# Kernel optimization log

Hardware: AMD Instinct MI355X
Metric: run time of the kernel (lower is better)

Reference implementation:

```python
import jax, jax.numpy as jnp
import numpy as np

B, S, D, H, F, E = 4, 1024, 1024, 16, 4096, 8
HD = D // H  # head dim


def setup_inputs() -> dict:
    key = jax.random.key(0)
    ks = jax.random.split(key, 8)
    p = lambda k, shp: jax.random.normal(k, shp, jnp.float32) * 0.02
    return {
        "x": jax.random.normal(ks[0], (B, S, D), jnp.float32),
        "mask": jnp.ones((B, S), jnp.int32),
        "in_proj_w": p(ks[1], (3 * D, D)),
        "in_proj_b": jnp.zeros((3 * D,), jnp.float32),
        "out_proj_w": p(ks[2], (D, D)),
        "out_proj_b": jnp.zeros((D,), jnp.float32),
        "ln1_g": jnp.ones((D,), jnp.float32),
        "ln1_b": jnp.zeros((D,), jnp.float32),
        "ln2_g": jnp.ones((D,), jnp.float32),
        "ln2_b": jnp.zeros((D,), jnp.float32),
        "gate_w": p(ks[3], (E, D)),
        "gate_b": jnp.zeros((E,), jnp.float32),
        "w1": p(ks[4], (E, F, D)),
        "b1": jnp.zeros((E, F), jnp.float32),
        "w2": p(ks[5], (E, D, F)),
        "b2": jnp.zeros((E, D), jnp.float32),
    }


def _layernorm(x, g, b, eps=1e-5):
    m = x.mean(-1, keepdims=True)
    v = ((x - m) ** 2).mean(-1, keepdims=True)
    return (x - m) / jnp.sqrt(v + eps) * g + b


def _mha(x, key_pad, in_proj_w, in_proj_b, out_proj_w, out_proj_b):
    # combined QKV projection as in torch nn.MultiheadAttention
    qkv = x @ in_proj_w.T + in_proj_b  # (B,S,3D)
    q, k, v = jnp.split(qkv, 3, axis=-1)
    def heads(t):
        return t.reshape(B, S, H, HD).transpose(0, 2, 1, 3)  # (B,H,S,HD)
    q, k, v = heads(q), heads(k), heads(v)
    scores = jnp.einsum("bhqd,bhkd->bhqk", q, k) / jnp.sqrt(jnp.float32(HD))
    scores = jnp.where(key_pad[:, None, None, :], -1e30, scores)
    attn = jax.nn.softmax(scores, axis=-1)
    out = jnp.einsum("bhqk,bhkd->bhqd", attn, v)  # (B,H,S,HD)
    out = out.transpose(0, 2, 1, 3).reshape(B, S, D)
    return out @ out_proj_w.T + out_proj_b


def _moe(x, gate_w, gate_b, w1, b1, w2, b2):
    logits = x @ gate_w.T + gate_b            # (B,S,E)
    probs = jax.nn.softmax(logits, axis=-1)
    # dense all-expert FFN (faithful to original: every expert computed)
    h = jax.nn.relu(jnp.einsum("bsd,efd->bsef", x, w1) + b1)   # (B,S,E,F)
    all_out = jnp.einsum("bsef,edf->bsed", h, w2) + b2          # (B,S,E,D)
    top_vals, top_idx = jax.lax.top_k(probs, 2)                 # (B,S,2)
    weights = top_vals / (top_vals.sum(-1, keepdims=True) + 1e-9)
    sel = jnp.take_along_axis(all_out, top_idx[..., None], axis=2)  # (B,S,2,D)
    return (sel * weights[..., None]).sum(axis=2)


def reference(x, mask, in_proj_w, in_proj_b, out_proj_w, out_proj_b,
              ln1_g, ln1_b, ln2_g, ln2_b, gate_w, gate_b, w1, b1, w2, b2):
    key_pad = mask == 0  # (B,S) bool
    attn_out = _mha(x, key_pad, in_proj_w, in_proj_b, out_proj_w, out_proj_b)
    x1 = _layernorm(x + attn_out, ln1_g, ln1_b)
    ff = _moe(x1, gate_w, gate_b, w1, b1, w2, b2)
    return _layernorm(x1 + ff, ln2_g, ln2_b)
```

## Files before the change

kernel.cpp:

```cpp
#include <hip/hip_runtime.h>

typedef __attribute__((ext_vector_type(8))) short bf16x8;
typedef __attribute__((ext_vector_type(4))) float f32x4;

#define DEV __device__ __forceinline__

static constexpr int Bb = 4, Sq = 1024, Dd = 1024, Hh = 16, HDd = 64, Ff = 4096, Ee = 8;
static constexpr int Nn = Bb * Sq;
static constexpr int TD = 3 * Dd;
static constexpr int PMAX = 2 * Nn + Ee * 256;

DEV unsigned short f2bf(float x) {
  union { float f; unsigned u; } c; c.f = x;
  unsigned r = c.u + 0x7FFFu + ((c.u >> 16) & 1u);
  return (unsigned short)(r >> 16);
}
DEV float bf2f(unsigned short u) {
  union { unsigned u; float f; } c; c.u = ((unsigned)u) << 16; return c.f;
}

typedef const __attribute__((address_space(1))) unsigned int* gas_t;
typedef __attribute__((address_space(3))) unsigned int* las_t;
DEV void gload16(const void* g, void* l) {
  __builtin_amdgcn_global_load_lds((gas_t)g, (las_t)l, 16, 0, 0);
}

__global__ __launch_bounds__(256) void cvt_kernel(const float* __restrict__ in,
                                                  unsigned short* __restrict__ out) {
  int i = blockIdx.x * 256 + threadIdx.x;
  const float4 a = *(const float4*)(in + (size_t)i * 8);
  const float4 b = *(const float4*)(in + (size_t)i * 8 + 4);
  union { uint4 u; unsigned short s[8]; } pk;
  pk.s[0] = f2bf(a.x); pk.s[1] = f2bf(a.y); pk.s[2] = f2bf(a.z); pk.s[3] = f2bf(a.w);
  pk.s[4] = f2bf(b.x); pk.s[5] = f2bf(b.y); pk.s[6] = f2bf(b.z); pk.s[7] = f2bf(b.w);
  *(uint4*)(out + (size_t)i * 8) = pk.u;
}

DEV void xcd_swz(int& bx, int& by, int gx, int gy) {
  const int nwg = gx * gy;
  int orig = by * gx + bx;
  int q = nwg >> 3, r = nwg & 7;
  int xcd = orig & 7, lin = orig >> 3;
  int wg = (xcd < r ? xcd * (q + 1) : r * (q + 1) + (xcd - r) * q) + lin;
  bx = wg / gy; by = wg % gy;
}

__global__ __launch_bounds__(512) void gemm8p_up(
    const unsigned short* __restrict__ A, const unsigned short* __restrict__ Bw,
    const float* __restrict__ bias, unsigned short* __restrict__ o0,
    const int* __restrict__ poff) {
  constexpr int K = Dd;
  constexpr int NT = K / 64;
  int bx = blockIdx.x, by = blockIdx.y;
  xcd_swz(bx, by, gridDim.x, gridDim.y);
  const int m0 = bx * 256;
  if (m0 >= poff[Ee]) return;
  int e = 0;
#pragma unroll
  for (int k = 1; k < Ee; ++k) if (m0 >= poff[k]) e = k;
  const int n0 = by * 256;
  const unsigned short* Bptr = Bw + (size_t)e * Ff * K;
  const float* biasptr = bias + e * Ff;

  __shared__ __align__(128) unsigned short As[2 * 256 * 64];
  __shared__ __align__(128) unsigned short Bs[2 * 256 * 64];

  const int tid = threadIdx.x;
  const int lane = tid & 63, wid = tid >> 6;
  const int aw = wid & 1, bw = wid >> 1;
  const int lr = lane & 15, lk = lane >> 4;

  const char* aS[2][2]; const char* bS[2][2]; int dOf[2];
#pragma unroll
  for (int it = 0; it < 2; ++it) {
    int b = it * 8192 + tid * 16;
    int r = b >> 7;
    int colb = (b & 127) ^ ((r & 7) << 4);
#pragma unroll
    for (int h = 0; h < 2; ++h) {
      aS[h][it] = (const char*)(A + (size_t)(m0 + h * 128 + r) * K) + colb;
      bS[h][it] = (const char*)(Bptr + (size_t)(n0 + h * 128 + r) * K) + colb;
    }
    dOf[it] = it * 8192 + wid * 1024;
  }
  int aO[2][2][4], bO[2][2][2];
#pragma unroll
  for (int h = 0; h < 2; ++h)
#pragma unroll
    for (int ks = 0; ks < 2; ++ks) {
#pragma unroll
      for (int mi = 0; mi < 4; ++mi) {
        int ra = h * 128 + aw * 64 + mi * 16 + lr;
        aO[h][ks][mi] = ra * 64 + (((ks * 4 + lk) ^ (ra & 7)) << 3);
      }
#pragma unroll
      for (int ni = 0; ni < 2; ++ni) {
        int rb = h * 128 + bw * 32 + ni * 16 + lr;
        bO[h][ks][ni] = rb * 64 + (((ks * 4 + lk) ^ (rb & 7)) << 3);
      }
    }

  f32x4 acc[4][4][2] = {};

  auto ST_A = [&](int t, int h) {
    int buf = t & 1;
#pragma unroll
    for (int it = 0; it < 2; ++it)
      gload16(aS[h][it] + (size_t)t * 128, (char*)As + buf * 32768 + h * 16384 + dOf[it]);
  };
  auto ST_B = [&](int t, int h) {
    int buf = t & 1;
#pragma unroll
    for (int it = 0; it < 2; ++it)
      gload16(bS[h][it] + (size_t)t * 128, (char*)Bs + buf * 32768 + h * 16384 + dOf[it]);
  };

  ST_A(0, 0); ST_B(0, 0); ST_B(0, 1); ST_A(0, 1);

  for (int t = 0; t < NT; ++t) {
    const unsigned short* Ab = As + (t & 1) * 16384;
    const unsigned short* Bb = Bs + (t & 1) * 16384;
#pragma unroll
    for (int p = 0; p < 4; ++p) {
      const int ah = p >> 1, bh = p & 1;
      if (t + 1 < NT) {
        if (p == 0)      ST_A(t + 1, 0);
        else if (p == 1) ST_B(t + 1, 0);
        else if (p == 2) ST_B(t + 1, 1);
        else             ST_A(t + 1, 1);
        asm volatile("s_waitcnt vmcnt(6)" ::: "memory");
      } else {
        if (p == 0)      asm volatile("s_waitcnt vmcnt(4)" ::: "memory");
        else if (p == 1) asm volatile("s_waitcnt vmcnt(2)" ::: "memory");
        else             asm volatile("s_waitcnt vmcnt(0)" ::: "memory");
      }
      __builtin_amdgcn_sched_barrier(0);
      asm volatile("s_barrier" ::: "memory");
      __builtin_amdgcn_sched_barrier(0);
      bf16x8 af[2][4], bf[2][2];
#pragma unroll
      for (int ks = 0; ks < 2; ++ks) {
#pragma unroll
        for (int mi = 0; mi < 4; ++mi) af[ks][mi] = *(const bf16x8*)&Ab[aO[ah][ks][mi]];
#pragma unroll
        for (int ni = 0; ni < 2; ++ni) bf[ks][ni] = *(const bf16x8*)&Bb[bO[bh][ks][ni]];
      }
      __builtin_amdgcn_s_setprio(1);
#pragma unroll
      for (int ks = 0; ks < 2; ++ks)
#pragma unroll
        for (int mi = 0; mi < 4; ++mi)
#pragma unroll
          for (int ni = 0; ni < 2; ++ni)
            acc[p][mi][ni] = __builtin_amdgcn_mfma_f32_16x16x32_bf16(af[ks][mi], bf[ks][ni], acc[p][mi][ni], 0, 0, 0);
      __builtin_amdgcn_s_setprio(0);
    }
  }

#pragma unroll
  for (int p = 0; p < 4; ++p)
#pragma unroll
    for (int ni = 0; ni < 2; ++ni) {
      const int col = n0 + (p & 1) * 128 + bw * 32 + ni * 16 + lr;
      const float bv = biasptr[col];
#pragma unroll
      for (int mi = 0; mi < 4; ++mi)
#pragma unroll
        for (int i = 0; i < 4; ++i) {
          const int row = m0 + (p >> 1) * 128 + aw * 64 + mi * 16 + lk * 4 + i;
          float v = acc[p][mi][ni][i] + bv;
          o0[(size_t)row * Ff + col] = f2bf(fmaxf(v, 0.f));
        }
    }
}

template <int EPI, int BM, int BN>
__global__ __launch_bounds__(256) void gemm_bt(
    const unsigned short* __restrict__ A, const unsigned short* __restrict__ Bw,
    const float* __restrict__ bias, void* __restrict__ o0, void* __restrict__ o1,
    void* __restrict__ o2, int M, int Ncols, int K,
    const int* __restrict__ poff) {
  constexpr int NA = BM / 64, NB = BN / 64;
  constexpr int L = NA + NB;
  constexpr int WM = BM / 2, WN = BN / 2;
  constexpr int MI = WM / 16, NI = WN / 16;
  constexpr int ATILE = BM * 32;
  constexpr int BTILE = BN * 32;

  int bx = blockIdx.x, by = blockIdx.y;
  xcd_swz(bx, by, gridDim.x, gridDim.y);
  const int m0 = bx * BM;
  int e = 0;
  if constexpr (EPI == 3) {
    if (m0 >= poff[Ee]) return;
#pragma unroll
    for (int k = 1; k < Ee; ++k) if (m0 >= poff[k]) e = k;
  } else {
    if (m0 >= M) return;
  }
  const int n0 = by * BN;
  const unsigned short* Bptr = Bw + (size_t)e * Ncols * K;
  const float* biasptr = bias + e * Ncols;

  __shared__ __align__(128) unsigned short As[3 * ATILE];
  __shared__ __align__(128) unsigned short Bs[3 * BTILE];

  const int tid = threadIdx.x;
  const int lane = tid & 63, wid = tid >> 6;
  const int wm = wid >> 1, wn = wid & 1;
  const int lr = lane & 15, lk = lane >> 4;

  const char* aSrc[NA]; const char* bSrc[NB];
  int aDf[NA], bDf[NB];
#pragma unroll
  for (int it = 0; it < NA; ++it) {
    int b = it * 4096 + tid * 16;
    int r = b >> 6;
    int colb = (b & 63) ^ (((r >> 1) & 3) << 4);
    aSrc[it] = (const char*)(A + (size_t)(m0 + r) * K) + colb;
    aDf[it] = it * 4096 + wid * 1024;
  }
#pragma unroll
  for (int it = 0; it < NB; ++it) {
    int b = it * 4096 + tid * 16;
    int r = b >> 6;
    int colb = (b & 63) ^ (((r >> 1) & 3) << 4);
    bSrc[it] = (const char*)(Bptr + (size_t)(n0 + r) * K) + colb;
    bDf[it] = it * 4096 + wid * 1024;
  }
  int aOff[MI], bOff[NI];
#pragma unroll
  for (int i = 0; i < MI; ++i) {
    int ra = wm * WM + i * 16 + lr;
    aOff[i] = ra * 32 + ((lk ^ ((ra >> 1) & 3)) << 3);
  }
#pragma unroll
  for (int i = 0; i < NI; ++i) {
    int rb = wn * WN + i * 16 + lr;
    bOff[i] = rb * 32 + ((lk ^ ((rb >> 1) & 3)) << 3);
  }

  auto STAGE = [&](int t, int buf) {
#pragma unroll
    for (int it = 0; it < NA; ++it)
      gload16(aSrc[it] + (size_t)t * 64, (char*)As + buf * (ATILE * 2) + aDf[it]);
#pragma unroll
    for (int it = 0; it < NB; ++it)
      gload16(bSrc[it] + (size_t)t * 64, (char*)Bs + buf * (BTILE * 2) + bDf[it]);
  };

  f32x4 acc[MI][NI] = {};
  const int NT = K >> 5;

  STAGE(0, 0);
  STAGE(1, 1);
  int cb = 0, sb = 2;
  for (int t = 0; t < NT; ++t) {
    if (t + 1 < NT) {
      if constexpr (L == 4)      asm volatile("s_waitcnt vmcnt(4)" ::: "memory");
      else if constexpr (L == 3) asm volatile("s_waitcnt vmcnt(3)" ::: "memory");
      else                       asm volatile("s_waitcnt vmcnt(2)" ::: "memory");
    } else {
      asm volatile("s_waitcnt vmcnt(0)" ::: "memory");
    }
    __builtin_amdgcn_sched_barrier(0);
    __builtin_amdgcn_s_barrier();
    __builtin_amdgcn_sched_barrier(0);
    if (t + 2 < NT) STAGE(t + 2, sb);
    const unsigned short* Ab = As + cb * ATILE;
    const unsigned short* Bb2 = Bs + cb * BTILE;
    bf16x8 af[MI], bfv[NI];
#pragma unroll
    for (int mi = 0; mi < MI; ++mi) af[mi] = *(const bf16x8*)&Ab[aOff[mi]];
#pragma unroll
    for (int ni = 0; ni < NI; ++ni) bfv[ni] = *(const bf16x8*)&Bb2[bOff[ni]];
#pragma unroll
    for (int mi = 0; mi < MI; ++mi)
#pragma unroll
      for (int ni = 0; ni < NI; ++ni)
        acc[mi][ni] = __builtin_amdgcn_mfma_f32_16x16x32_bf16(af[mi], bfv[ni], acc[mi][ni], 0, 0, 0);
    cb = (cb == 2) ? 0 : cb + 1;
    sb = (sb == 2) ? 0 : sb + 1;
  }

#pragma unroll
  for (int ni = 0; ni < NI; ++ni) {
    const int col = n0 + wn * WN + ni * 16 + lr;
    const float bv = biasptr[col];
#pragma unroll
    for (int mi = 0; mi < MI; ++mi) {
#pragma unroll
      for (int i = 0; i < 4; ++i) {
        const int mloc = wm * WM + mi * 16 + lk * 4 + i;
        float v = acc[mi][ni][i] + bv;
        if constexpr (EPI == 0) {
          int t = m0 + mloc;
          int which = col >> 10, jj = col & 1023, hh = jj >> 6, hd = jj & 63;
          int bb = t >> 10, s = t & 1023;
          unsigned short* dst = (which == 0) ? (unsigned short*)o0
                              : (which == 1) ? (unsigned short*)o1 : (unsigned short*)o2;
          dst[((size_t)(bb * Hh + hh) * Sq + s) * HDd + hd] = f2bf(v);
        } else if constexpr (EPI == 1) {
          ((float*)o0)[(size_t)(m0 + mloc) * Dd + col] = v;
        } else {
          ((unsigned short*)o0)[(size_t)(m0 + mloc) * Dd + col] = f2bf(v);
        }
      }
    }
  }
}

__global__ __launch_bounds__(256) void attn_kernel(
    const unsigned short* __restrict__ qb, const unsigned short* __restrict__ kb,
    const unsigned short* __restrict__ vb, const int* __restrict__ mask,
    unsigned short* __restrict__ attnb) {
  const int qt = blockIdx.x, h = blockIdx.y, b = blockIdx.z;
  const unsigned short* Q = qb + (size_t)(b * Hh + h) * Sq * HDd;
  const unsigned short* Kg = kb + (size_t)(b * Hh + h) * Sq * HDd;
  const unsigned short* Vg = vb + (size_t)(b * Hh + h) * Sq * HDd;

  __shared__ unsigned short Qs[64 * 72], Ks[64 * 72], Vt[64 * 72], Ps[64 * 72];
  __shared__ float Ssm[64 * 65];
  __shared__ float mS[64], lS[64], aS[64];
  __shared__ int mk[64];

  const int tid = threadIdx.x, lane = tid & 63, wid = tid >> 6;
  const int lr = lane & 15, lk = lane >> 4;

#pragma unroll
  for (int it = 0; it < 2; ++it) {
    int c = tid + it * 256; int r = c >> 3, kc = (c & 7) * 8;
    *(uint4*)&Qs[r * 72 + kc] = *(const uint4*)(Q + (size_t)(qt * 64 + r) * 64 + kc);
  }
  if (tid < 64) { mS[tid] = -1e30f; lS[tid] = 0.f; }

  f32x4 oacc[4] = {};

  for (int kt = 0; kt < 16; ++kt) {
    __syncthreads();
#pragma unroll
    for (int it = 0; it < 2; ++it) {
      int c = tid + it * 256; int r = c >> 3, kc = (c & 7) * 8;
      *(uint4*)&Ks[r * 72 + kc] = *(const uint4*)(Kg + (size_t)(kt * 64 + r) * 64 + kc);
    }
    {
      int kk = tid >> 2, hg = (tid & 3) * 16;
      union { uint4 u[2]; unsigned short s[16]; } tv;
      tv.u[0] = *(const uint4*)(Vg + (size_t)(kt * 64 + kk) * 64 + hg);
      tv.u[1] = *(const uint4*)(Vg + (size_t)(kt * 64 + kk) * 64 + hg + 8);
#pragma unroll
      for (int j = 0; j < 16; ++j) Vt[(hg + j) * 72 + kk] = tv.s[j];
    }
    if (tid < 64) mk[tid] = mask[b * Sq + kt * 64 + tid];
    __syncthreads();

    f32x4 sacc[4] = {};
#pragma unroll
    for (int ks = 0; ks < 2; ++ks) {
      bf16x8 aq = *(const bf16x8*)&Qs[(wid * 16 + lr) * 72 + ks * 32 + lk * 8];
#pragma unroll
      for (int ni = 0; ni < 4; ++ni) {
        bf16x8 bk = *(const bf16x8*)&Ks[(ni * 16 + lr) * 72 + ks * 32 + lk * 8];
        sacc[ni] = __builtin_amdgcn_mfma_f32_16x16x32_bf16(aq, bk, sacc[ni], 0, 0, 0);
      }
    }
#pragma unroll
    for (int ni = 0; ni < 4; ++ni)
#pragma unroll
      for (int i = 0; i < 4; ++i) {
        int r = wid * 16 + lk * 4 + i, cc = ni * 16 + lr;
        float v = sacc[ni][i] * 0.125f;
        if (mk[cc] == 0) v = -1e30f;
        Ssm[r * 65 + cc] = v;
      }
    __syncthreads();
    {
      int r = tid >> 2, cg = (tid & 3) * 16;
      float xv[16];
#pragma unroll
      for (int j = 0; j < 16; ++j) xv[j] = Ssm[r * 65 + cg + j];
      float mx = xv[0];
#pragma unroll
      for (int j = 1; j < 16; ++j) mx = fmaxf(mx, xv[j]);
      mx = fmaxf(mx, __shfl_xor(mx, 1));
      mx = fmaxf(mx, __shfl_xor(mx, 2));
      float mprev = mS[r];
      float mnew = fmaxf(mprev, mx);
      float sum = 0.f;
      union { uint4 u[2]; unsigned short s[16]; } pb;
#pragma unroll
      for (int j = 0; j < 16; ++j) {
        float pv = expf(xv[j] - mnew);
        sum += pv; pb.s[j] = f2bf(pv);
      }
      sum += __shfl_xor(sum, 1);
      sum += __shfl_xor(sum, 2);
      *(uint4*)&Ps[r * 72 + cg] = pb.u[0];
      *(uint4*)&Ps[r * 72 + cg + 8] = pb.u[1];
      if ((tid & 3) == 0) {
        float alpha = expf(mprev - mnew);
        mS[r] = mnew; aS[r] = alpha; lS[r] = lS[r] * alpha + sum;
      }
    }
    __syncthreads();
#pragma unroll
    for (int ni = 0; ni < 4; ++ni)
#pragma unroll
      for (int i = 0; i < 4; ++i)
        oacc[ni][i] *= aS[wid * 16 + lk * 4 + i];
#pragma unroll
    for (int ks = 0; ks < 2; ++ks) {
      bf16x8 ap = *(const bf16x8*)&Ps[(wid * 16 + lr) * 72 + ks * 32 + lk * 8];
#pragma unroll
      for (int ni = 0; ni < 4; ++ni) {
        bf16x8 bv = *(const bf16x8*)&Vt[(ni * 16 + lr) * 72 + ks * 32 + lk * 8];
        oacc[ni] = __builtin_amdgcn_mfma_f32_16x16x32_bf16(ap, bv, oacc[ni], 0, 0, 0);
      }
    }
  }
  __syncthreads();
#pragma unroll
  for (int ni = 0; ni < 4; ++ni)
#pragma unroll
    for (int i = 0; i < 4; ++i) {
      int r = wid * 16 + lk * 4 + i;
      int q = qt * 64 + r;
      float v = oacc[ni][i] / lS[r];
      attnb[((size_t)(b * Sq + q)) * Dd + h * 64 + ni * 16 + lr] = f2bf(v);
    }
}

__global__ __launch_bounds__(256) void ln1_route_kernel(
    const float* __restrict__ a, const float* __restrict__ b2,
    const float* __restrict__ g, const float* __restrict__ beta,
    const float* __restrict__ gw, const float* __restrict__ gb,
    float* __restrict__ outf, unsigned short* __restrict__ outb,
    int* __restrict__ cnt, int* __restrict__ tokslot, float* __restrict__ wtok) {
  const int t = blockIdx.x, tid = threadIdx.x;
  float4 v = *(const float4*)(a + (size_t)t * Dd + tid * 4);
  {
    float4 u = *(const float4*)(b2 + (size_t)t * Dd + tid * 4);
    v.x += u.x; v.y += u.y; v.z += u.z; v.w += u.w;
  }
  const int lane = tid & 63, wid = tid >> 6;
  float s = v.x + v.y + v.z + v.w;
  for (int sh = 1; sh < 64; sh <<= 1) s += __shfl_xor(s, sh);
  __shared__ float red[4], red2[4];
  __shared__ float gred[4 * Ee];
  if (lane == 0) red[wid] = s;
  __syncthreads();
  float mean = (red[0] + red[1] + red[2] + red[3]) * (1.f / Dd);
  float dx = v.x - mean, dy = v.y - mean, dz = v.z - mean, dw = v.w - mean;
  float q = dx * dx + dy * dy + dz * dz + dw * dw;
  for (int sh = 1; sh < 64; sh <<= 1) q += __shfl_xor(q, sh);
  if (lane == 0) red2[wid] = q;
  __syncthreads();
  float var = (red2[0] + red2[1] + red2[2] + red2[3]) * (1.f / Dd);
  float rstd = rsqrtf(var + 1e-5f);
  float4 gg = *(const float4*)(g + tid * 4);
  float4 bbv = *(const float4*)(beta + tid * 4);
  float4 o;
  o.x = dx * rstd * gg.x + bbv.x;
  o.y = dy * rstd * gg.y + bbv.y;
  o.z = dz * rstd * gg.z + bbv.z;
  o.w = dw * rstd * gg.w + bbv.w;
  *(float4*)(outf + (size_t)t * Dd + tid * 4) = o;
  {
    ushort4 pk; pk.x = f2bf(o.x); pk.y = f2bf(o.y); pk.z = f2bf(o.z); pk.w = f2bf(o.w);
    *(ushort4*)(outb + (size_t)t * Dd + tid * 4) = pk;
  }
  float gacc[Ee];
#pragma unroll
  for (int e = 0; e < Ee; ++e) {
    float4 gv = *(const float4*)(gw + (size_t)e * Dd + tid * 4);
    gacc[e] = o.x * gv.x + o.y * gv.y + o.z * gv.z + o.w * gv.w;
  }
#pragma unroll
  for (int e = 0; e < Ee; ++e)
    for (int sh = 1; sh < 64; sh <<= 1) gacc[e] += __shfl_xor(gacc[e], sh);
  if (lane == 0) {
#pragma unroll
    for (int e = 0; e < Ee; ++e) gred[wid * Ee + e] = gacc[e];
  }
  __syncthreads();
  if (tid == 0) {
    float lg[Ee];
#pragma unroll
    for (int e = 0; e < Ee; ++e)
      lg[e] = gred[e] + gred[Ee + e] + gred[2 * Ee + e] + gred[3 * Ee + e] + gb[e];
    float m = lg[0];
#pragma unroll
    for (int e = 1; e < Ee; ++e) m = fmaxf(m, lg[e]);
    float p[Ee], ssum = 0.f;
#pragma unroll
    for (int e = 0; e < Ee; ++e) { p[e] = expf(lg[e] - m); ssum += p[e]; }
    int e0 = 0;
#pragma unroll
    for (int e = 1; e < Ee; ++e) if (p[e] > p[e0]) e0 = e;
    int e1 = -1;
#pragma unroll
    for (int e = 0; e < Ee; ++e) {
      if (e == e0) continue;
      if (e1 < 0 || p[e] > p[e1]) e1 = e;
    }
    float v0 = p[e0] / ssum, v1 = p[e1] / ssum;
    float wsum = v0 + v1 + 1e-9f;
    wtok[t * 2] = v0 / wsum; wtok[t * 2 + 1] = v1 / wsum;
    int p0 = atomicAdd(&cnt[e0], 1);
    tokslot[e0 * Nn + p0] = t * 2;
    int p1 = atomicAdd(&cnt[e1], 1);
    tokslot[e1 * Nn + p1] = t * 2 + 1;
  }
}

__global__ __launch_bounds__(256) void ln2_kernel(
    const float* __restrict__ x1f, const unsigned short* __restrict__ ffp,
    const int* __restrict__ inv, const float* __restrict__ wtok,
    const float* __restrict__ g, const float* __restrict__ beta,
    float* __restrict__ out) {
  const int t = blockIdx.x, tid = threadIdx.x;
  const int i0 = inv[2 * t], i1 = inv[2 * t + 1];
  const float w0 = wtok[2 * t], w1 = wtok[2 * t + 1];
  float4 v = *(const float4*)(x1f + (size_t)t * Dd + tid * 4);
  ushort4 u0 = *(const ushort4*)(ffp + (size_t)i0 * Dd + tid * 4);
  ushort4 u1 = *(const ushort4*)(ffp + (size_t)i1 * Dd + tid * 4);
  v.x += w0 * bf2f(u0.x) + w1 * bf2f(u1.x);
  v.y += w0 * bf2f(u0.y) + w1 * bf2f(u1.y);
  v.z += w0 * bf2f(u0.z) + w1 * bf2f(u1.z);
  v.w += w0 * bf2f(u0.w) + w1 * bf2f(u1.w);
  const int lane = tid & 63, wid = tid >> 6;
  float s = v.x + v.y + v.z + v.w;
  for (int sh = 1; sh < 64; sh <<= 1) s += __shfl_xor(s, sh);
  __shared__ float red[4], red2[4];
  if (lane == 0) red[wid] = s;
  __syncthreads();
  float mean = (red[0] + red[1] + red[2] + red[3]) * (1.f / Dd);
  float dx = v.x - mean, dy = v.y - mean, dz = v.z - mean, dw = v.w - mean;
  float q = dx * dx + dy * dy + dz * dz + dw * dw;
  for (int sh = 1; sh < 64; sh <<= 1) q += __shfl_xor(q, sh);
  if (lane == 0) red2[wid] = q;
  __syncthreads();
  float var = (red2[0] + red2[1] + red2[2] + red2[3]) * (1.f / Dd);
  float rstd = rsqrtf(var + 1e-5f);
  float4 gg = *(const float4*)(g + tid * 4);
  float4 bb = *(const float4*)(beta + tid * 4);
  float4 o;
  o.x = dx * rstd * gg.x + bb.x;
  o.y = dy * rstd * gg.y + bb.y;
  o.z = dz * rstd * gg.z + bb.z;
  o.w = dw * rstd * gg.w + bb.w;
  *(float4*)(out + (size_t)t * Dd + tid * 4) = o;
}

__global__ void offsets_kernel(const int* __restrict__ cnt, int* __restrict__ poff) {
  if (threadIdx.x == 0) {
    int s = 0;
    for (int e = 0; e < Ee; ++e) { poff[e] = s; s += (cnt[e] + 255) & ~255; }
    poff[Ee] = s;
  }
}

__global__ __launch_bounds__(256) void pack_kernel(
    const unsigned short* __restrict__ x1b, const int* __restrict__ tokslot,
    const int* __restrict__ cnt, const int* __restrict__ poff,
    unsigned short* __restrict__ xg, int* __restrict__ inv) {
  const int tid = threadIdx.x;
  const int g = blockIdx.x * 8 + (tid >> 5);
  const int l = tid & 31;
  if (g >= poff[Ee]) return;
  int e = 0;
#pragma unroll
  for (int k = 1; k < Ee; ++k) if (g >= poff[k]) e = k;
  const int pos = g - poff[e];
  uint4* dst = (uint4*)(xg + (size_t)g * Dd);
  if (pos < cnt[e]) {
    const int ent = tokslot[e * Nn + pos];
    if (l == 0) inv[ent] = g;
    const uint4* src = (const uint4*)(x1b + (size_t)(ent >> 1) * Dd);
#pragma unroll
    for (int j = 0; j < 4; ++j) dst[l + j * 32] = src[l + j * 32];
  } else {
    const uint4 z = make_uint4(0, 0, 0, 0);
#pragma unroll
    for (int j = 0; j < 4; ++j) dst[l + j * 32] = z;
  }
}

extern "C" void kernel_launch(void* const* d_in, const int* in_sizes, int n_in,
                              void* d_out, int out_size, void* d_ws, size_t ws_size,
                              hipStream_t stream) {
  const float* x   = (const float*)d_in[0];
  const int*   msk = (const int*)d_in[1];
  const float* ipw = (const float*)d_in[2];
  const float* ipb = (const float*)d_in[3];
  const float* opw = (const float*)d_in[4];
  const float* opb = (const float*)d_in[5];
  const float* g1  = (const float*)d_in[6];
  const float* be1 = (const float*)d_in[7];
  const float* g2  = (const float*)d_in[8];
  const float* be2 = (const float*)d_in[9];
  const float* gw  = (const float*)d_in[10];
  const float* gb  = (const float*)d_in[11];
  const float* w1  = (const float*)d_in[12];
  const float* b1  = (const float*)d_in[13];
  const float* w2  = (const float*)d_in[14];
  const float* b2  = (const float*)d_in[15];
  float* out = (float*)d_out;

  char* p = (char*)d_ws;
  auto carve = [&](size_t bytes) { char* r = p; p += (bytes + 255) & ~(size_t)255; return r; };
  unsigned short* xb   = (unsigned short*)carve((size_t)Nn * Dd * 2);
  unsigned short* qb   = (unsigned short*)carve((size_t)Nn * Dd * 2);
  unsigned short* kb   = (unsigned short*)carve((size_t)Nn * Dd * 2);
  unsigned short* vb   = (unsigned short*)carve((size_t)Nn * Dd * 2);
  float* proj          = (float*)carve((size_t)Nn * Dd * 4);
  float* x1f           = (float*)carve((size_t)Nn * Dd * 4);
  unsigned short* x1b  = (unsigned short*)carve((size_t)Nn * Dd * 2);
  unsigned short* xg   = (unsigned short*)carve((size_t)PMAX * Dd * 2);
  unsigned short* ffp  = (unsigned short*)carve((size_t)PMAX * Dd * 2);
  unsigned short* hbuf = (unsigned short*)carve((size_t)PMAX * Ff * 2);
  unsigned short* wbuf = (unsigned short*)carve((size_t)Ee * Ff * Dd * 2);
  int* cnt             = (int*)carve(64);
  int* poff            = (int*)carve(64);
  int* tokslot         = (int*)carve((size_t)Ee * Nn * 4);
  float* wtok          = (float*)carve((size_t)2 * Nn * 4);
  int* inv             = (int*)carve((size_t)2 * Nn * 4);
  unsigned short* attnb = xb;

  cvt_kernel<<<Nn * Dd / 2048, 256, 0, stream>>>(x, xb);
  cvt_kernel<<<TD * Dd / 2048, 256, 0, stream>>>(ipw, wbuf);
  gemm_bt<0, 128, 64><<<dim3(Nn / 128, TD / 64), 256, 0, stream>>>(
      xb, wbuf, ipb, qb, kb, vb, Nn, TD, Dd, nullptr);
  attn_kernel<<<dim3(Sq / 64, Hh, Bb), 256, 0, stream>>>(qb, kb, vb, msk, attnb);
  cvt_kernel<<<Dd * Dd / 2048, 256, 0, stream>>>(opw, wbuf);
  gemm_bt<1, 64, 64><<<dim3(Nn / 64, Dd / 64), 256, 0, stream>>>(
      attnb, wbuf, opb, proj, nullptr, nullptr, Nn, Dd, Dd, nullptr);
  hipMemsetAsync(cnt, 0, 64, stream);
  ln1_route_kernel<<<Nn, 256, 0, stream>>>(x, proj, g1, be1, gw, gb,
                                           x1f, x1b, cnt, tokslot, wtok);
  offsets_kernel<<<1, 64, 0, stream>>>(cnt, poff);
  pack_kernel<<<PMAX / 8, 256, 0, stream>>>(x1b, tokslot, cnt, poff, xg, inv);
  cvt_kernel<<<Ee * Ff * Dd / 2048, 256, 0, stream>>>(w1, wbuf);
  gemm8p_up<<<dim3(PMAX / 256, Ff / 256), 512, 0, stream>>>(xg, wbuf, b1, hbuf, poff);
  cvt_kernel<<<Ee * Dd * Ff / 2048, 256, 0, stream>>>(w2, wbuf);
  gemm_bt<3, 128, 128><<<dim3(PMAX / 128, Dd / 128), 256, 0, stream>>>(
      hbuf, wbuf, b2, ffp, nullptr, nullptr, PMAX, Dd, Ff, poff);
  ln2_kernel<<<Nn, 256, 0, stream>>>(x1f, ffp, inv, wtok, g2, be2, out);
}
```

Measured before the change: 612.7 us.

## Fuse fp32-to-bf16 weight conversion into MoE expert GEMMs, drop separate cvt passes

The MoE up and down GEMMs now read the fp32 expert weights directly. Each tile is converted to bf16 in registers and written to shared memory inside a software pipeline, so the two full-weight cvt kernels and their bf16 staging buffer are no longer needed. The specialised 256x256 512-thread up-projection kernel is removed, and the up GEMM reuses the generic 128x128 template with a ReLU epilogue. This saves roughly 256MB of weight write-and-reread traffic. The cost is twice the global read volume per weight tile, extra VALU conversion work, and weights re-read and re-converted by every M-tile.

```diff
diff --git a/kernel.cpp b/kernel.cpp
--- a/kernel.cpp
+++ b/kernel.cpp
@@ -45,153 +45,25 @@
   bx = wg / gy; by = wg % gy;
 }
 
-__global__ __launch_bounds__(512) void gemm8p_up(
-    const unsigned short* __restrict__ A, const unsigned short* __restrict__ Bw,
-    const float* __restrict__ bias, unsigned short* __restrict__ o0,
-    const int* __restrict__ poff) {
-  constexpr int K = Dd;
-  constexpr int NT = K / 64;
-  int bx = blockIdx.x, by = blockIdx.y;
-  xcd_swz(bx, by, gridDim.x, gridDim.y);
-  const int m0 = bx * 256;
-  if (m0 >= poff[Ee]) return;
-  int e = 0;
-#pragma unroll
-  for (int k = 1; k < Ee; ++k) if (m0 >= poff[k]) e = k;
-  const int n0 = by * 256;
-  const unsigned short* Bptr = Bw + (size_t)e * Ff * K;
-  const float* biasptr = bias + e * Ff;
-
-  __shared__ __align__(128) unsigned short As[2 * 256 * 64];
-  __shared__ __align__(128) unsigned short Bs[2 * 256 * 64];
-
-  const int tid = threadIdx.x;
-  const int lane = tid & 63, wid = tid >> 6;
-  const int aw = wid & 1, bw = wid >> 1;
-  const int lr = lane & 15, lk = lane >> 4;
-
-  const char* aS[2][2]; const char* bS[2][2]; int dOf[2];
-#pragma unroll
-  for (int it = 0; it < 2; ++it) {
-    int b = it * 8192 + tid * 16;
-    int r = b >> 7;
-    int colb = (b & 127) ^ ((r & 7) << 4);
-#pragma unroll
-    for (int h = 0; h < 2; ++h) {
-      aS[h][it] = (const char*)(A + (size_t)(m0 + h * 128 + r) * K) + colb;
-      bS[h][it] = (const char*)(Bptr + (size_t)(n0 + h * 128 + r) * K) + colb;
-    }
-    dOf[it] = it * 8192 + wid * 1024;
-  }
-  int aO[2][2][4], bO[2][2][2];
-#pragma unroll
-  for (int h = 0; h < 2; ++h)
-#pragma unroll
-    for (int ks = 0; ks < 2; ++ks) {
-#pragma unroll
-      for (int mi = 0; mi < 4; ++mi) {
-        int ra = h * 128 + aw * 64 + mi * 16 + lr;
-        aO[h][ks][mi] = ra * 64 + (((ks * 4 + lk) ^ (ra & 7)) << 3);
-      }
-#pragma unroll
-      for (int ni = 0; ni < 2; ++ni) {
-        int rb = h * 128 + bw * 32 + ni * 16 + lr;
-        bO[h][ks][ni] = rb * 64 + (((ks * 4 + lk) ^ (rb & 7)) << 3);
-      }
-    }
-
-  f32x4 acc[4][4][2] = {};
-
-  auto ST_A = [&](int t, int h) {
-    int buf = t & 1;
-#pragma unroll
-    for (int it = 0; it < 2; ++it)
-      gload16(aS[h][it] + (size_t)t * 128, (char*)As + buf * 32768 + h * 16384 + dOf[it]);
-  };
-  auto ST_B = [&](int t, int h) {
-    int buf = t & 1;
-#pragma unroll
-    for (int it = 0; it < 2; ++it)
-      gload16(bS[h][it] + (size_t)t * 128, (char*)Bs + buf * 32768 + h * 16384 + dOf[it]);
-  };
-
-  ST_A(0, 0); ST_B(0, 0); ST_B(0, 1); ST_A(0, 1);
-
-  for (int t = 0; t < NT; ++t) {
-    const unsigned short* Ab = As + (t & 1) * 16384;
-    const unsigned short* Bb = Bs + (t & 1) * 16384;
-#pragma unroll
-    for (int p = 0; p < 4; ++p) {
-      const int ah = p >> 1, bh = p & 1;
-      if (t + 1 < NT) {
-        if (p == 0)      ST_A(t + 1, 0);
-        else if (p == 1) ST_B(t + 1, 0);
-        else if (p == 2) ST_B(t + 1, 1);
-        else             ST_A(t + 1, 1);
-        asm volatile("s_waitcnt vmcnt(6)" ::: "memory");
-      } else {
-        if (p == 0)      asm volatile("s_waitcnt vmcnt(4)" ::: "memory");
-        else if (p == 1) asm volatile("s_waitcnt vmcnt(2)" ::: "memory");
-        else             asm volatile("s_waitcnt vmcnt(0)" ::: "memory");
-      }
-      __builtin_amdgcn_sched_barrier(0);
-      asm volatile("s_barrier" ::: "memory");
-      __builtin_amdgcn_sched_barrier(0);
-      bf16x8 af[2][4], bf[2][2];
-#pragma unroll
-      for (int ks = 0; ks < 2; ++ks) {
-#pragma unroll
-        for (int mi = 0; mi < 4; ++mi) af[ks][mi] = *(const bf16x8*)&Ab[aO[ah][ks][mi]];
-#pragma unroll
-        for (int ni = 0; ni < 2; ++ni) bf[ks][ni] = *(const bf16x8*)&Bb[bO[bh][ks][ni]];
-      }
-      __builtin_amdgcn_s_setprio(1);
-#pragma unroll
-      for (int ks = 0; ks < 2; ++ks)
-#pragma unroll
-        for (int mi = 0; mi < 4; ++mi)
-#pragma unroll
-          for (int ni = 0; ni < 2; ++ni)
-            acc[p][mi][ni] = __builtin_amdgcn_mfma_f32_16x16x32_bf16(af[ks][mi], bf[ks][ni], acc[p][mi][ni], 0, 0, 0);
-      __builtin_amdgcn_s_setprio(0);
-    }
-  }
-
-#pragma unroll
-  for (int p = 0; p < 4; ++p)
-#pragma unroll
-    for (int ni = 0; ni < 2; ++ni) {
-      const int col = n0 + (p & 1) * 128 + bw * 32 + ni * 16 + lr;
-      const float bv = biasptr[col];
-#pragma unroll
-      for (int mi = 0; mi < 4; ++mi)
-#pragma unroll
-        for (int i = 0; i < 4; ++i) {
-          const int row = m0 + (p >> 1) * 128 + aw * 64 + mi * 16 + lk * 4 + i;
-          float v = acc[p][mi][ni][i] + bv;
-          o0[(size_t)row * Ff + col] = f2bf(fmaxf(v, 0.f));
-        }
-    }
-}
-
-template <int EPI, int BM, int BN>
+template <int EPI, int BM, int BN, bool BF32>
 __global__ __launch_bounds__(256) void gemm_bt(
-    const unsigned short* __restrict__ A, const unsigned short* __restrict__ Bw,
-    const float* __restrict__ bias, void* __restrict__ o0, void* __restrict__ o1,
-    void* __restrict__ o2, int M, int Ncols, int K,
-    const int* __restrict__ poff) {
+    const unsigned short* __restrict__ A, const unsigned short* __restrict__ Bw16,
+    const float* __restrict__ Bw32, const float* __restrict__ bias,
+    void* __restrict__ o0, void* __restrict__ o1, void* __restrict__ o2,
+    int M, int Ncols, int K, const int* __restrict__ poff) {
   constexpr int NA = BM / 64, NB = BN / 64;
   constexpr int L = NA + NB;
   constexpr int WM = BM / 2, WN = BN / 2;
   constexpr int MI = WM / 16, NI = WN / 16;
   constexpr int ATILE = BM * 32;
   constexpr int BTILE = BN * 32;
+  static_assert(!BF32 || (BM == 128 && BN == 128), "BF32 path assumes 128x128");
 
   int bx = blockIdx.x, by = blockIdx.y;
   xcd_swz(bx, by, gridDim.x, gridDim.y);
   const int m0 = bx * BM;
   int e = 0;
-  if constexpr (EPI == 3) {
+  if constexpr (EPI >= 2) {
     if (m0 >= poff[Ee]) return;
 #pragma unroll
     for (int k = 1; k < Ee; ++k) if (m0 >= poff[k]) e = k;
@@ -199,7 +71,6 @@
     if (m0 >= M) return;
   }
   const int n0 = by * BN;
-  const unsigned short* Bptr = Bw + (size_t)e * Ncols * K;
   const float* biasptr = bias + e * Ncols;
 
   __shared__ __align__(128) unsigned short As[3 * ATILE];
@@ -210,8 +81,7 @@
   const int wm = wid >> 1, wn = wid & 1;
   const int lr = lane & 15, lk = lane >> 4;
 
-  const char* aSrc[NA]; const char* bSrc[NB];
-  int aDf[NA], bDf[NB];
+  const char* aSrc[NA]; int aDf[NA];
 #pragma unroll
   for (int it = 0; it < NA; ++it) {
     int b = it * 4096 + tid * 16;
@@ -220,14 +90,6 @@
     aSrc[it] = (const char*)(A + (size_t)(m0 + r) * K) + colb;
     aDf[it] = it * 4096 + wid * 1024;
   }
-#pragma unroll
-  for (int it = 0; it < NB; ++it) {
-    int b = it * 4096 + tid * 16;
-    int r = b >> 6;
-    int colb = (b & 63) ^ (((r >> 1) & 3) << 4);
-    bSrc[it] = (const char*)(Bptr + (size_t)(n0 + r) * K) + colb;
-    bDf[it] = it * 4096 + wid * 1024;
-  }
   int aOff[MI], bOff[NI];
 #pragma unroll
   for (int i = 0; i < MI; ++i) {
@@ -240,47 +102,120 @@
     bOff[i] = rb * 32 + ((lk ^ ((rb >> 1) & 3)) << 3);
   }
 
-  auto STAGE = [&](int t, int buf) {
+  auto ST_A = [&](int t, int buf) {
 #pragma unroll
     for (int it = 0; it < NA; ++it)
       gload16(aSrc[it] + (size_t)t * 64, (char*)As + buf * (ATILE * 2) + aDf[it]);
-#pragma unroll
-    for (int it = 0; it < NB; ++it)
-      gload16(bSrc[it] + (size_t)t * 64, (char*)Bs + buf * (BTILE * 2) + bDf[it]);
   };
 
   f32x4 acc[MI][NI] = {};
   const int NT = K >> 5;
 
-  STAGE(0, 0);
-  STAGE(1, 1);
-  int cb = 0, sb = 2;
-  for (int t = 0; t < NT; ++t) {
-    if (t + 1 < NT) {
-      if constexpr (L == 4)      asm volatile("s_waitcnt vmcnt(4)" ::: "memory");
-      else if constexpr (L == 3) asm volatile("s_waitcnt vmcnt(3)" ::: "memory");
-      else                       asm volatile("s_waitcnt vmcnt(2)" ::: "memory");
-    } else {
-      asm volatile("s_waitcnt vmcnt(0)" ::: "memory");
-    }
-    __builtin_amdgcn_sched_barrier(0);
-    __builtin_amdgcn_s_barrier();
-    __builtin_amdgcn_sched_barrier(0);
-    if (t + 2 < NT) STAGE(t + 2, sb);
-    const unsigned short* Ab = As + cb * ATILE;
-    const unsigned short* Bb2 = Bs + cb * BTILE;
-    bf16x8 af[MI], bfv[NI];
-#pragma unroll
-    for (int mi = 0; mi < MI; ++mi) af[mi] = *(const bf16x8*)&Ab[aOff[mi]];
-#pragma unroll
-    for (int ni = 0; ni < NI; ++ni) bfv[ni] = *(const bf16x8*)&Bb2[bOff[ni]];
-#pragma unroll
-    for (int mi = 0; mi < MI; ++mi)
-#pragma unroll
-      for (int ni = 0; ni < NI; ++ni)
-        acc[mi][ni] = __builtin_amdgcn_mfma_f32_16x16x32_bf16(af[mi], bfv[ni], acc[mi][ni], 0, 0, 0);
-    cb = (cb == 2) ? 0 : cb + 1;
-    sb = (sb == 2) ? 0 : sb + 1;
+  if constexpr (!BF32) {
+    const unsigned short* Bptr = Bw16 + (size_t)e * Ncols * K;
+    const char* bSrc[NB]; int bDf[NB];
+#pragma unroll
+    for (int it = 0; it < NB; ++it) {
+      int b = it * 4096 + tid * 16;
+      int r = b >> 6;
+      int colb = (b & 63) ^ (((r >> 1) & 3) << 4);
+      bSrc[it] = (const char*)(Bptr + (size_t)(n0 + r) * K) + colb;
+      bDf[it] = it * 4096 + wid * 1024;
+    }
+    auto STAGE = [&](int t, int buf) {
+      ST_A(t, buf);
+#pragma unroll
+      for (int it = 0; it < NB; ++it)
+        gload16(bSrc[it] + (size_t)t * 64, (char*)Bs + buf * (BTILE * 2) + bDf[it]);
+    };
+    STAGE(0, 0);
+    STAGE(1, 1);
+    int cb = 0, sb = 2;
+    for (int t = 0; t < NT; ++t) {
+      if (t + 1 < NT) {
+        if constexpr (L == 4)      asm volatile("s_waitcnt vmcnt(4)" ::: "memory");
+        else if constexpr (L == 3) asm volatile("s_waitcnt vmcnt(3)" ::: "memory");
+        else                       asm volatile("s_waitcnt vmcnt(2)" ::: "memory");
+      } else {
+        asm volatile("s_waitcnt vmcnt(0)" ::: "memory");
+      }
+      __builtin_amdgcn_sched_barrier(0);
+      __builtin_amdgcn_s_barrier();
+      __builtin_amdgcn_sched_barrier(0);
+      if (t + 2 < NT) STAGE(t + 2, sb);
+      const unsigned short* Ab = As + cb * ATILE;
+      const unsigned short* Bb2 = Bs + cb * BTILE;
+      bf16x8 af[MI], bfv[NI];
+#pragma unroll
+      for (int mi = 0; mi < MI; ++mi) af[mi] = *(const bf16x8*)&Ab[aOff[mi]];
+#pragma unroll
+      for (int ni = 0; ni < NI; ++ni) bfv[ni] = *(const bf16x8*)&Bb2[bOff[ni]];
+#pragma unroll
+      for (int mi = 0; mi < MI; ++mi)
+#pragma unroll
+        for (int ni = 0; ni < NI; ++ni)
+          acc[mi][ni] = __builtin_amdgcn_mfma_f32_16x16x32_bf16(af[mi], bfv[ni], acc[mi][ni], 0, 0, 0);
+      cb = (cb == 2) ? 0 : cb + 1;
+      sb = (sb == 2) ? 0 : sb + 1;
+    }
+  } else {
+    const int br = tid >> 1;
+    const int bh = tid & 1;
+    const float* bF = Bw32 + (size_t)e * Ncols * K + (size_t)(n0 + br) * K + bh * 16;
+    const int bw0 = br * 32 + (((2 * bh) ^ ((br >> 1) & 3)) << 3);
+    const int bw1 = br * 32 + (((2 * bh + 1) ^ ((br >> 1) & 3)) << 3);
+
+    float4 rA[4], rB[4];
+    auto LD_B = [&](int t, float4 (&r)[4]) {
+      const float* s = bF + (size_t)t * 32;
+      r[0] = *(const float4*)(s);     r[1] = *(const float4*)(s + 4);
+      r[2] = *(const float4*)(s + 8); r[3] = *(const float4*)(s + 12);
+    };
+    auto WR_B = [&](int buf, const float4 (&r)[4]) {
+      union { uint4 u; unsigned short s[8]; } p0, p1;
+      p0.s[0] = f2bf(r[0].x); p0.s[1] = f2bf(r[0].y); p0.s[2] = f2bf(r[0].z); p0.s[3] = f2bf(r[0].w);
+      p0.s[4] = f2bf(r[1].x); p0.s[5] = f2bf(r[1].y); p0.s[6] = f2bf(r[1].z); p0.s[7] = f2bf(r[1].w);
+      p1.s[0] = f2bf(r[2].x); p1.s[1] = f2bf(r[2].y); p1.s[2] = f2bf(r[2].z); p1.s[3] = f2bf(r[2].w);
+      p1.s[4] = f2bf(r[3].x); p1.s[5] = f2bf(r[3].y); p1.s[6] = f2bf(r[3].z); p1.s[7] = f2bf(r[3].w);
+      *(uint4*)&Bs[buf * BTILE + bw0] = p0.u;
+      *(uint4*)&Bs[buf * BTILE + bw1] = p1.u;
+    };
+
+    LD_B(0, rA); ST_A(0, 0); LD_B(1, rB); ST_A(1, 1);
+    WR_B(0, rA);
+
+    int cb = 0, sb = 2;
+    auto BODY = [&](int t, float4 (&wset)[4], float4 (&lset)[4]) {
+      if (t + 1 < NT) asm volatile("s_waitcnt vmcnt(6) lgkmcnt(0)" ::: "memory");
+      else            asm volatile("s_waitcnt vmcnt(0) lgkmcnt(0)" ::: "memory");
+      __builtin_amdgcn_sched_barrier(0);
+      __builtin_amdgcn_s_barrier();
+      __builtin_amdgcn_sched_barrier(0);
+      if (t + 2 < NT) { LD_B(t + 2, lset); ST_A(t + 2, sb); }
+      __builtin_amdgcn_sched_barrier(0);
+      if (t + 1 < NT) {
+        int nb = (cb == 2) ? 0 : cb + 1;
+        WR_B(nb, wset);
+      }
+      const unsigned short* Ab = As + cb * ATILE;
+      const unsigned short* Bb2 = Bs + cb * BTILE;
+      bf16x8 af[MI], bfv[NI];
+#pragma unroll
+      for (int mi = 0; mi < MI; ++mi) af[mi] = *(const bf16x8*)&Ab[aOff[mi]];
+#pragma unroll
+      for (int ni = 0; ni < NI; ++ni) bfv[ni] = *(const bf16x8*)&Bb2[bOff[ni]];
+#pragma unroll
+      for (int mi = 0; mi < MI; ++mi)
+#pragma unroll
+        for (int ni = 0; ni < NI; ++ni)
+          acc[mi][ni] = __builtin_amdgcn_mfma_f32_16x16x32_bf16(af[mi], bfv[ni], acc[mi][ni], 0, 0, 0);
+      cb = (cb == 2) ? 0 : cb + 1;
+      sb = (sb == 2) ? 0 : sb + 1;
+    };
+    for (int t2 = 0; t2 < NT; t2 += 2) {
+      BODY(t2, rB, rA);
+      BODY(t2 + 1, rA, rB);
+    }
   }
 
 #pragma unroll
@@ -302,6 +237,8 @@
           dst[((size_t)(bb * Hh + hh) * Sq + s) * HDd + hd] = f2bf(v);
         } else if constexpr (EPI == 1) {
           ((float*)o0)[(size_t)(m0 + mloc) * Dd + col] = v;
+        } else if constexpr (EPI == 2) {
+          ((unsigned short*)o0)[(size_t)(m0 + mloc) * (size_t)Ncols + col] = f2bf(fmaxf(v, 0.f));
         } else {
           ((unsigned short*)o0)[(size_t)(m0 + mloc) * Dd + col] = f2bf(v);
         }
@@ -619,7 +556,7 @@
   unsigned short* xg   = (unsigned short*)carve((size_t)PMAX * Dd * 2);
   unsigned short* ffp  = (unsigned short*)carve((size_t)PMAX * Dd * 2);
   unsigned short* hbuf = (unsigned short*)carve((size_t)PMAX * Ff * 2);
-  unsigned short* wbuf = (unsigned short*)carve((size_t)Ee * Ff * Dd * 2);
+  unsigned short* wbuf = (unsigned short*)carve((size_t)TD * Dd * 2);
   int* cnt             = (int*)carve(64);
   int* poff            = (int*)carve(64);
   int* tokslot         = (int*)carve((size_t)Ee * Nn * 4);
@@ -629,21 +566,20 @@
 
   cvt_kernel<<<Nn * Dd / 2048, 256, 0, stream>>>(x, xb);
   cvt_kernel<<<TD * Dd / 2048, 256, 0, stream>>>(ipw, wbuf);
-  gemm_bt<0, 128, 64><<<dim3(Nn / 128, TD / 64), 256, 0, stream>>>(
-      xb, wbuf, ipb, qb, kb, vb, Nn, TD, Dd, nullptr);
+  gemm_bt<0, 128, 64, false><<<dim3(Nn / 128, TD / 64), 256, 0, stream>>>(
+      xb, wbuf, nullptr, ipb, qb, kb, vb, Nn, TD, Dd, nullptr);
   attn_kernel<<<dim3(Sq / 64, Hh, Bb), 256, 0, stream>>>(qb, kb, vb, msk, attnb);
   cvt_kernel<<<Dd * Dd / 2048, 256, 0, stream>>>(opw, wbuf);
-  gemm_bt<1, 64, 64><<<dim3(Nn / 64, Dd / 64), 256, 0, stream>>>(
-      attnb, wbuf, opb, proj, nullptr, nullptr, Nn, Dd, Dd, nullptr);
+  gemm_bt<1, 64, 64, false><<<dim3(Nn / 64, Dd / 64), 256, 0, stream>>>(
+      attnb, wbuf, nullptr, opb, proj, nullptr, nullptr, Nn, Dd, Dd, nullptr);
   hipMemsetAsync(cnt, 0, 64, stream);
   ln1_route_kernel<<<Nn, 256, 0, stream>>>(x, proj, g1, be1, gw, gb,
                                            x1f, x1b, cnt, tokslot, wtok);
   offsets_kernel<<<1, 64, 0, stream>>>(cnt, poff);
   pack_kernel<<<PMAX / 8, 256, 0, stream>>>(x1b, tokslot, cnt, poff, xg, inv);
-  cvt_kernel<<<Ee * Ff * Dd / 2048, 256, 0, stream>>>(w1, wbuf);
-  gemm8p_up<<<dim3(PMAX / 256, Ff / 256), 512, 0, stream>>>(xg, wbuf, b1, hbuf, poff);
-  cvt_kernel<<<Ee * Dd * Ff / 2048, 256, 0, stream>>>(w2, wbuf);
-  gemm_bt<3, 128, 128><<<dim3(PMAX / 128, Dd / 128), 256, 0, stream>>>(
-      hbuf, wbuf, b2, ffp, nullptr, nullptr, PMAX, Dd, Ff, poff);
+  gemm_bt<2, 128, 128, true><<<dim3(PMAX / 128, Ff / 128), 256, 0, stream>>>(
+      xg, nullptr, w1, b1, hbuf, nullptr, nullptr, PMAX, Ff, Dd, poff);
+  gemm_bt<3, 128, 128, true><<<dim3(PMAX / 128, Dd / 128), 256, 0, stream>>>(
+      hbuf, nullptr, w2, b2, ffp, nullptr, nullptr, PMAX, Dd, Ff, poff);
   ln2_kernel<<<Nn, 256, 0, stream>>>(x1f, ffp, inv, wtok, g2, be2, out);
 }
```

Measured after the change: 797.6 us. 30.2% more time.
